# Optimization experiments

Hardware: AMD Instinct MI355X
Metric: run time of the kernel (lower is better)

## Reference

```python
import jax, jax.numpy as jnp
import numpy as np

N_NODES = 20000
N_EDGES = 320000
F_IN = 256      # feature_size
H1, C1 = 8, 128 # conv1: heads=8, out=128, concat -> 1024
H2, C2 = 1, 128 # conv2: heads=1, out=emb_size, concat=False
NEG_SLOPE = 0.2


def setup_inputs() -> dict:
    key = jax.random.key(0)
    ks = jax.random.split(key, 10)
    x = jax.random.normal(ks[0], (N_NODES, F_IN), dtype=jnp.float32)
    edge_index = jax.random.randint(ks[1], (2, N_EDGES), 0, N_NODES, dtype=jnp.int64)
    s1 = 1.0 / np.sqrt(F_IN)
    s2 = 1.0 / np.sqrt(H1 * C1)
    W1 = jax.random.uniform(ks[2], (F_IN, H1 * C1), jnp.float32, -s1, s1)
    att_src1 = jax.random.uniform(ks[3], (H1, C1), jnp.float32, -s1, s1)
    att_dst1 = jax.random.uniform(ks[4], (H1, C1), jnp.float32, -s1, s1)
    bias1 = jnp.zeros((H1 * C1,), jnp.float32)
    W2 = jax.random.uniform(ks[5], (H1 * C1, H2 * C2), jnp.float32, -s2, s2)
    att_src2 = jax.random.uniform(ks[6], (H2, C2), jnp.float32, -s2, s2)
    att_dst2 = jax.random.uniform(ks[7], (H2, C2), jnp.float32, -s2, s2)
    bias2 = jnp.zeros((C2,), jnp.float32)
    return {"x": x, "edge_index": edge_index,
            "W1": W1, "att_src1": att_src1, "att_dst1": att_dst1, "bias1": bias1,
            "W2": W2, "att_src2": att_src2, "att_dst2": att_dst2, "bias2": bias2}


def _gat_conv(x, W, a_src, a_dst, bias, src, dst, num_nodes, concat):
    """PyG-style GATConv (eval mode, self-loops already appended to src/dst)."""
    H, C = a_src.shape
    h = (x @ W).reshape(num_nodes, H, C)                     # [N,H,C]
    alpha_src = jnp.sum(h * a_src[None], axis=-1)            # [N,H]
    alpha_dst = jnp.sum(h * a_dst[None], axis=-1)            # [N,H]
    e = alpha_src[src] + alpha_dst[dst]                      # [E,H]
    e = jnp.where(e > 0, e, NEG_SLOPE * e)                   # LeakyReLU(0.2)
    # segment softmax over incoming edges of each dst node
    m = jax.ops.segment_max(e, dst, num_segments=num_nodes)  # [N,H]
    ex = jnp.exp(e - m[dst])
    denom = jax.ops.segment_sum(ex, dst, num_segments=num_nodes)
    alpha = ex / (denom[dst] + 1e-16)                        # [E,H]
    msg = alpha[:, :, None] * h[src]                         # [E,H,C]
    out = jax.ops.segment_sum(msg, dst, num_segments=num_nodes)  # [N,H,C]
    if concat:
        out = out.reshape(num_nodes, H * C)
    else:
        out = out.mean(axis=1)
    return out + bias


def reference(x, edge_index, W1, att_src1, att_dst1, bias1, W2, att_src2, att_dst2, bias2):
    n = x.shape[0]
    loop = jnp.arange(n, dtype=edge_index.dtype)
    src = jnp.concatenate([edge_index[0], loop])
    dst = jnp.concatenate([edge_index[1], loop])
    # dropout layers are identity in eval mode
    h = _gat_conv(x, W1, att_src1, att_dst1, bias1, src, dst, n, concat=True)
    h = jax.nn.elu(h)
    h = _gat_conv(h, W2, att_src2, att_dst2, bias2, src, dst, n, concat=False)
    return jax.nn.log_softmax(h, axis=-1)
```

## Files before the change

kernel.cpp:

```cpp
#include <hip/hip_runtime.h>

#define NN 20000
#define FIN 256
#define D1 1024
#define NH 8
#define C2 128
#define CAP 64

typedef unsigned short u16;
typedef unsigned char u8;
typedef __attribute__((ext_vector_type(8))) short bf16x8;
typedef __attribute__((ext_vector_type(4))) float f32x4;
typedef __attribute__((ext_vector_type(2))) float f32x2;

__device__ __forceinline__ float bf2f(u16 u) {
    return __uint_as_float(((unsigned int)u) << 16);
}
__device__ __forceinline__ u16 f2bf(float f) {
    unsigned int u = __float_as_uint(f);
    u += 0x7FFFu + ((u >> 16) & 1u);
    return (u16)(u >> 16);
}
__device__ __forceinline__ u8 f2fp8(float v) {
    int q = __builtin_amdgcn_cvt_pk_fp8_f32(v, v, 0, false);
    return (u8)(q & 0xFF);
}

__device__ __forceinline__ float bred_max(float v) {
    #pragma unroll
    for (int o = 32; o > 0; o >>= 1) v = fmaxf(v, __shfl_xor(v, o, 64));
    return v;
}
__device__ __forceinline__ float bred_sum(float v) {
    #pragma unroll
    for (int o = 32; o > 0; o >>= 1) v += __shfl_xor(v, o, 64);
    return v;
}

typedef const __attribute__((address_space(1))) unsigned int* as1_u32p;
typedef __attribute__((address_space(3))) unsigned int* as3_u32p;
__device__ __forceinline__ void gload_lds16(const void* g, void* l) {
    __builtin_amdgcn_global_load_lds((as1_u32p)g, (as3_u32p)l, 16, 0, 0);
}

__global__ __launch_bounds__(256) void prep_kernel(const float* __restrict__ x,
                                                   u16* __restrict__ xb,
                                                   const float* __restrict__ W1,
                                                   u16* __restrict__ w1t,
                                                   const float* __restrict__ W2,
                                                   u16* __restrict__ w2t,
                                                   int* __restrict__ cnt) {
    __shared__ float tile[32][33];
    const int b = blockIdx.x, tid = threadIdx.x;
    if (b < 5000) {
        int i = (b * 256 + tid) * 4;
        if (i < NN * FIN) {
            float4 v = *(const float4*)(x + i);
            ushort4 o;
            o.x = f2bf(v.x); o.y = f2bf(v.y); o.z = f2bf(v.z); o.w = f2bf(v.w);
            *(ushort4*)(xb + i) = o;
        }
        return;
    }
    if (b < 5384) {
        const float* in; u16* out; int R, C, bx, by;
        if (b < 5256) {
            int q = b - 5000;
            in = W1; out = w1t; R = FIN; C = D1;
            bx = (q & 31) * 32; by = (q >> 5) * 32;
        } else {
            int q = b - 5256;
            in = W2; out = w2t; R = D1; C = C2;
            bx = (q & 3) * 32; by = (q >> 2) * 32;
        }
        int tx = tid & 31, ty = tid >> 5;
        #pragma unroll
        for (int i = 0; i < 32; i += 8)
            tile[ty + i][tx] = in[(size_t)(by + ty + i) * C + bx + tx];
        __syncthreads();
        #pragma unroll
        for (int i = 0; i < 32; i += 8)
            out[(size_t)(bx + ty + i) * R + by + tx] = f2bf(tile[tx][ty + i]);
        return;
    }
    int i = (b - 5384) * 256 + tid;
    if (i < NN) cnt[i] = 0;
}

#define G_STAGE(BUF, K0)                                                   \
    {                                                                      \
        _Pragma("unroll")                                                  \
        for (int i = 0; i < BM / 64; i++) {                                \
            int c = tid + i * 256;                                         \
            int r = c >> 2, ko = (c & 3) * 8;                              \
            int gr = row0 + r; if (gr >= M) gr = M - 1;                    \
            gload_lds16(A + (size_t)gr * K + (K0) + ko,                    \
                        &ldsA[BUF][c * 8]);                                \
        }                                                                  \
        _Pragma("unroll")                                                  \
        for (int i = 0; i < 2; i++) {                                      \
            int c = tid + i * 256;                                         \
            int n = c >> 2, ko = (c & 3) * 8;                              \
            gload_lds16(Bt + (size_t)(col0 + n) * K + (K0) + ko,           \
                        &ldsB[BUF][c * 8]);                                \
        }                                                                  \
    }

template <int BM, int OMODE>
__global__ __launch_bounds__(256) void gemm_mfma(const u16* __restrict__ A,
                                                 const u16* __restrict__ Bt,
                                                 void* __restrict__ C,
                                                 const float* __restrict__ attS,
                                                 const float* __restrict__ attD,
                                                 float* __restrict__ as_out,
                                                 float* __restrict__ ad_out,
                                                 int NHo,
                                                 int M, int N, int K) {
    constexpr int TM = BM / 32;
    __shared__ u16 ldsA[2][BM * 32];
    __shared__ u16 ldsB[2][128 * 32];
    __shared__ float asb[BM], adb[BM];
    const int tid = threadIdx.x;
    const int lane = tid & 63, w = tid >> 6;
    const int wr = w >> 1, wc = w & 1;
    const int row0 = blockIdx.x * BM, col0 = blockIdx.y * 128;
    const int head = blockIdx.y;
    const int l15 = lane & 15, quad = lane >> 4;

    for (int t = tid; t < BM; t += 256) { asb[t] = 0.f; adb[t] = 0.f; }

    f32x4 acc[TM][4];
    #pragma unroll
    for (int i = 0; i < TM; i++)
        #pragma unroll
        for (int j = 0; j < 4; j++)
            acc[i][j] = (f32x4){0.f, 0.f, 0.f, 0.f};

    G_STAGE(0, 0)
    __syncthreads();
    int cur = 0;
    for (int k0 = 0; k0 < K; k0 += 32) {
        if (k0 + 32 < K) {
            G_STAGE(cur ^ 1, k0 + 32)
            __builtin_amdgcn_sched_barrier(0);
        }
        bf16x8 af[TM], bfr[4];
        #pragma unroll
        for (int i = 0; i < TM; i++) {
            int m = wr * (BM / 2) + i * 16 + l15;
            af[i] = *(const bf16x8*)(&ldsA[cur][m * 32 + quad * 8]);
        }
        #pragma unroll
        for (int j = 0; j < 4; j++) {
            int n = wc * 64 + j * 16 + l15;
            bfr[j] = *(const bf16x8*)(&ldsB[cur][n * 32 + quad * 8]);
        }
        #pragma unroll
        for (int i = 0; i < TM; i++)
            #pragma unroll
            for (int j = 0; j < 4; j++)
                acc[i][j] = __builtin_amdgcn_mfma_f32_16x16x32_bf16(af[i], bfr[j], acc[i][j], 0, 0, 0);
        __syncthreads();
        cur ^= 1;
    }
    #pragma unroll
    for (int i = 0; i < TM; i++) {
        #pragma unroll
        for (int j = 0; j < 4; j++) {
            #pragma unroll
            for (int r = 0; r < 4; r++) {
                int row = row0 + wr * (BM / 2) + i * 16 + quad * 4 + r;
                int col = col0 + wc * 64 + j * 16 + l15;
                if (row < M) {
                    float v = acc[i][j][r];
                    if (OMODE == 1)
                        ((u16*)C)[(size_t)row * N + col] = f2bf(v);
                    else
                        ((u8*)C)[(size_t)row * N + col] = f2fp8(v);
                }
            }
        }
    }
    float attS_r[4], attD_r[4];
    #pragma unroll
    for (int j = 0; j < 4; j++) {
        int col = wc * 64 + j * 16 + l15;
        attS_r[j] = attS[head * 128 + col];
        attD_r[j] = attD[head * 128 + col];
    }
    #pragma unroll
    for (int i = 0; i < TM; i++) {
        #pragma unroll
        for (int r = 0; r < 4; r++) {
            float ps = 0.f, pd = 0.f;
            #pragma unroll
            for (int j = 0; j < 4; j++) {
                float v = acc[i][j][r];
                ps = fmaf(v, attS_r[j], ps);
                pd = fmaf(v, attD_r[j], pd);
            }
            #pragma unroll
            for (int o = 1; o < 16; o <<= 1) {
                ps += __shfl_xor(ps, o, 64);
                pd += __shfl_xor(pd, o, 64);
            }
            if (l15 == 0) {
                int row = wr * (BM / 2) + i * 16 + quad * 4 + r;
                atomicAdd(&asb[row], ps);
                atomicAdd(&adb[row], pd);
            }
        }
    }
    __syncthreads();
    for (int t = tid; t < BM; t += 256) {
        int row = row0 + t;
        if (row < M) {
            as_out[(size_t)row * NHo + head] = asb[t];
            ad_out[(size_t)row * NHo + head] = adb[t];
        }
    }
}

__global__ void fill_kernel(const int* __restrict__ ei, int E, int N,
                            int* __restrict__ cnt,
                            int* __restrict__ csr) {
    int j = blockIdx.x * 256 + threadIdx.x;
    if (j >= E + N) return;
    int s, d;
    if (j < E) { s = ei[j]; d = ei[E + j]; }
    else { s = j - E; d = j - E; }
    int pos = atomicAdd(&cnt[d], 1);
    if (pos >= CAP) return;
    csr[d * CAP + pos] = s;
}

#define A1_FETCH8(E0, Q, P)                                                   \
    {                                                                         \
        _Pragma("unroll")                                                     \
        for (int u = 0; u < 8; u++) {                                         \
            int e = (E0) + u;                       \
            int s = __builtin_amdgcn_readlane(idx, e);                        \
            s = s < 0 ? 0 : (s > NN - 1 ? NN - 1 : s);        \
            Q[u] = *(const uint4*)(h1q + (size_t)s * D1 + c0);                \
            P[u] = as1[s * NH + h];            \
        }                                                                     \
        __builtin_amdgcn_sched_barrier(0);                                    \
    }
#define A1_PROC8(E0, Q, P)                                                    \
    {                                                                         \
        _Pragma("unroll")                                                     \
        for (int u = 0; u < 8; u++) {                                         \
            float ev = (P)[u] + adv;                                          \
            ev = ev > 0.f ? ev : 0.2f * ev;               \
            float pp = ((E0) + u < deg) ? __expf(ev) : 0.f;                   \
            den += pp;                                                        \
            f32x2 pv2 = {pp, pp};                                             \
            acc[0] += pv2 * __builtin_amdgcn_cvt_pk_f32_fp8((Q)[u].x, false); \
            acc[1] += pv2 * __builtin_amdgcn_cvt_pk_f32_fp8((Q)[u].x, true);  \
            acc[2] += pv2 * __builtin_amdgcn_cvt_pk_f32_fp8((Q)[u].y, false); \
            acc[3] += pv2 * __builtin_amdgcn_cvt_pk_f32_fp8((Q)[u].y, true);  \
            acc[4] += pv2 * __builtin_amdgcn_cvt_pk_f32_fp8((Q)[u].z, false); \
            acc[5] += pv2 * __builtin_amdgcn_cvt_pk_f32_fp8((Q)[u].z, true);  \
            acc[6] += pv2 * __builtin_amdgcn_cvt_pk_f32_fp8((Q)[u].w, false); \
            acc[7] += pv2 * __builtin_amdgcn_cvt_pk_f32_fp8((Q)[u].w, true);  \
        }                                                                     \
    }

__global__ __launch_bounds__(256) void agg1_kernel(const u8* __restrict__ h1q,
                                                   const float* __restrict__ as1,
                                                   const float* __restrict__ ad1,
                                                   const int* __restrict__ cnt,
                                                   const int* __restrict__ csr,
                                                   const float* __restrict__ bias1,
                                                   u16* __restrict__ x2) {
    const int tid = threadIdx.x;
    const int lane = tid & 63;
    const int dst = (blockIdx.x << 2) + (tid >> 6);
    const int c0 = lane * 16;
    const int h = lane >> 3;
    const int base = dst * CAP;

    int idx = csr[base + lane];
    const int deg = __builtin_amdgcn_readfirstlane(max(1, min(cnt[dst], CAP)));
    const float adv = ad1[dst * NH + h];

    f32x2 acc[8];
    #pragma unroll
    for (int k = 0; k < 8; k++) acc[k] = (f32x2){0.f, 0.f};
    float den = 0.f;

    const int nit = (deg + 7) >> 3;
    uint4 qa[8], qb[8];
    float pa[8], pb[8];
    A1_FETCH8(0, qa, pa)
    int g = 0;
    for (; g + 2 < nit; g += 2) {
        A1_FETCH8((g + 1) * 8, qb, pb)
        A1_PROC8(g * 8, qa, pa)
        A1_FETCH8((g + 2) * 8, qa, pa)
        A1_PROC8((g + 1) * 8, qb, pb)
    }
    if (g + 1 < nit) {
        A1_FETCH8((g + 1) * 8, qb, pb)
        A1_PROC8(g * 8, qa, pa)
        A1_PROC8((g + 1) * 8, qb, pb)
    } else {
        A1_PROC8(g * 8, qa, pa)
    }

    float inv = 1.f / (den + 1e-16f);
    u16 ov[16];
    #pragma unroll
    for (int k = 0; k < 8; k++) {
        float a0 = acc[k][0] * inv + bias1[c0 + 2 * k];
        float a1 = acc[k][1] * inv + bias1[c0 + 2 * k + 1];
        a0 = a0 > 0.f ? a0 : (__expf(a0) - 1.f);
        a1 = a1 > 0.f ? a1 : (__expf(a1) - 1.f);
        ov[2 * k] = f2bf(a0);
        ov[2 * k + 1] = f2bf(a1);
    }
    *(uint4*)(x2 + (size_t)dst * D1 + c0) = *(const uint4*)ov;
    *(uint4*)(x2 + (size_t)dst * D1 + c0 + 8) = *(const uint4*)(ov + 8);
}

#define A2_FETCH8(E0, Q)                                                      \
    {                                                                         \
        _Pragma("unroll")                                                     \
        for (int u = 0; u < 8; u++) {                                         \
            int s = __builtin_amdgcn_readlane(idx, (E0) + u);                 \
            s = s < 0 ? 0 : (s > NN - 1 ? NN - 1 : s);                        \
            Q[u] = *(const unsigned int*)(h2 + (size_t)s * C2 + lane2);       \
        }                                                                     \
        __builtin_amdgcn_sched_barrier(0);                                    \
    }
#define A2_PROC8(E0, Q)                                                       \
    {                                                                         \
        _Pragma("unroll")                                                     \
        for (int u = 0; u < 8; u++) {                                         \
            int e = (E0) + u;                                                 \
            float pp = (e < deg) ? __uint_as_float(__builtin_amdgcn_readlane( \
                                       __float_as_uint(pl), e))               \
                                 : 0.f;                                       \
            den += pp;                                                        \
            f32x2 pv2 = {pp, pp};                                             \
            f32x2 f = {__uint_as_float((Q)[u] << 16),                         \
                       __uint_as_float((Q)[u] & 0xFFFF0000u)};                \
            acc += pv2 * f;                                                   \
        }                                                                     \
    }

__global__ __launch_bounds__(256) void agg2_kernel(const u16* __restrict__ h2,
                                                   const float* __restrict__ as2,
                                                   const float* __restrict__ ad2,
                                                   const int* __restrict__ cnt,
                                                   const int* __restrict__ csr,
                                                   const float* __restrict__ bias2,
                                                   float* __restrict__ out) {
    const int tid = threadIdx.x;
    const int lane = tid & 63;
    const int dst = (blockIdx.x << 2) + (tid >> 6);
    const int base = dst * CAP;
    const int lane2 = lane * 2;

    int idx = csr[base + lane];
    const int deg = __builtin_amdgcn_readfirstlane(max(1, min(cnt[dst], CAP)));
    const float adv = ad2[dst];
    int idxc = idx < 0 ? 0 : (idx > NN - 1 ? NN - 1 : idx);
    float ev = as2[idxc] + adv;
    ev = ev > 0.f ? ev : 0.2f * ev;
    float pl = __expf(ev);

    f32x2 acc = {0.f, 0.f};
    float den = 0.f;

    const int nit = (deg + 7) >> 3;
    unsigned int qa[8], qb[8];
    A2_FETCH8(0, qa)
    int g = 0;
    for (; g + 2 < nit; g += 2) {
        A2_FETCH8((g + 1) * 8, qb)
        A2_PROC8(g * 8, qa)
        A2_FETCH8((g + 2) * 8, qa)
        A2_PROC8((g + 1) * 8, qb)
    }
    if (g + 1 < nit) {
        A2_FETCH8((g + 1) * 8, qb)
        A2_PROC8(g * 8, qa)
        A2_PROC8((g + 1) * 8, qb)
    } else {
        A2_PROC8(g * 8, qa)
    }

    float inv = 1.f / (den + 1e-16f);
    float l0 = acc[0] * inv + bias2[lane2];
    float l1 = acc[1] * inv + bias2[lane2 + 1];
    float m = bred_max(fmaxf(l0, l1));
    float ex = bred_sum(__expf(l0 - m) + __expf(l1 - m));
    float lse = m + __logf(ex);
    float2 ov = {l0 - lse, l1 - lse};
    *(float2*)(out + (size_t)dst * C2 + lane2) = ov;
}

extern "C" void kernel_launch(void* const* d_in, const int* in_sizes, int n_in,
                              void* d_out, int out_size, void* d_ws, size_t ws_size,
                              hipStream_t stream) {
    const float* x        = (const float*)d_in[0];
    const int*   ei       = (const int*)d_in[1];
    const float* W1       = (const float*)d_in[2];
    const float* att_src1 = (const float*)d_in[3];
    const float* att_dst1 = (const float*)d_in[4];
    const float* bias1    = (const float*)d_in[5];
    const float* W2       = (const float*)d_in[6];
    const float* att_src2 = (const float*)d_in[7];
    const float* att_dst2 = (const float*)d_in[8];
    const float* bias2    = (const float*)d_in[9];
    float* out = (float*)d_out;
    const int E = in_sizes[1] / 2;

    char* ws = (char*)d_ws;
    size_t off = 0;
    auto alloc = [&](size_t b) {
        void* p = ws + off;
        off += (b + 255) & ~(size_t)255;
        return p;
    };
    u8*  h1q  = (u8*)alloc((size_t)NN * D1);
    u16* x2   = (u16*)alloc((size_t)NN * D1 * 2);
    u16* h2   = (u16*)alloc((size_t)NN * C2 * 2);
    u16* xb   = (u16*)alloc((size_t)NN * FIN * 2);
    u16* w1t  = (u16*)alloc((size_t)D1 * FIN * 2);
    u16* w2t  = (u16*)alloc((size_t)C2 * D1 * 2);
    float* as1 = (float*)alloc((size_t)NN * NH * 4);
    float* ad1 = (float*)alloc((size_t)NN * NH * 4);
    float* as2 = (float*)alloc((size_t)NN * 4);
    float* ad2 = (float*)alloc((size_t)NN * 4);
    int* cnt  = (int*)alloc((size_t)NN * 4);
    int* csr  = (int*)alloc((size_t)NN * CAP * 4);

    const int PREP_BLOCKS = 5000 + 256 + 128 + (NN + 255) / 256;
    prep_kernel<<<PREP_BLOCKS, 256, 0, stream>>>(x, xb, W1, w1t, W2, w2t, cnt);

    gemm_mfma<128, 2><<<dim3((NN + 127) / 128, D1 / 128), 256, 0, stream>>>(
        xb, w1t, h1q, att_src1, att_dst1, as1, ad1, NH, NN, D1, FIN);
    fill_kernel<<<(E + NN + 255) / 256, 256, 0, stream>>>(ei, E, NN, cnt, csr);
    agg1_kernel<<<(NN + 3) / 4, 256, 0, stream>>>(h1q, as1, ad1, cnt, csr, bias1, x2);
    gemm_mfma<64, 1><<<dim3((NN + 63) / 64, C2 / 128), 256, 0, stream>>>(
        x2, w2t, h2, att_src2, att_dst2, as2, ad2, 1, NN, C2, D1);
    agg2_kernel<<<(NN + 3) / 4, 256, 0, stream>>>(h2, as2, ad2, cnt, csr, bias2, out);
}
```

Baseline: 231.2 us.

## Split layer-1 aggregation per head and fuse CSR fill into prep kernel

Layer-1 aggregation now launches 8x more blocks, one per (dst-group, head). Each wave handles one head's 128 columns, with each lane gathering 2 fp8 values per edge. Each lane computes one edge's attention weight up front, and the weights are broadcast with readlane, so per-edge exp and as1 loads are no longer repeated. The CSR fill kernel is folded into the prep kernel, and cnt is zeroed by a memset instead. The per-head split aims to raise parallelism and occupancy, but each gather is now a narrow 2-byte load and the csr/cnt reads are repeated eight times per node.

Result: slower. 260.0 us (+12.5%).

```diff
diff --git a/kernel.cpp b/kernel.cpp
--- a/kernel.cpp
+++ b/kernel.cpp
@@ -49,7 +49,10 @@
                                                    u16* __restrict__ w1t,
                                                    const float* __restrict__ W2,
                                                    u16* __restrict__ w2t,
-                                                   int* __restrict__ cnt) {
+                                                   const int* __restrict__ ei,
+                                                   int E,
+                                                   int* __restrict__ cnt,
+                                                   int* __restrict__ csr) {
     __shared__ float tile[32][33];
     const int b = blockIdx.x, tid = threadIdx.x;
     if (b < 5000) {
@@ -83,8 +86,14 @@
             out[(size_t)(bx + ty + i) * R + by + tx] = f2bf(tile[tx][ty + i]);
         return;
     }
-    int i = (b - 5384) * 256 + tid;
-    if (i < NN) cnt[i] = 0;
+    int j = (b - 5384) * 256 + tid;
+    if (j >= E + NN) return;
+    int s, d;
+    if (j < E) { s = ei[j]; d = ei[E + j]; }
+    else { s = j - E; d = j - E; }
+    int pos = atomicAdd(&cnt[d], 1);
+    if (pos >= CAP) return;
+    csr[d * CAP + pos] = s;
 }
 
 #define G_STAGE(BUF, K0)                                                   \
@@ -221,48 +230,28 @@
     }
 }
 
-__global__ void fill_kernel(const int* __restrict__ ei, int E, int N,
-                            int* __restrict__ cnt,
-                            int* __restrict__ csr) {
-    int j = blockIdx.x * 256 + threadIdx.x;
-    if (j >= E + N) return;
-    int s, d;
-    if (j < E) { s = ei[j]; d = ei[E + j]; }
-    else { s = j - E; d = j - E; }
-    int pos = atomicAdd(&cnt[d], 1);
-    if (pos >= CAP) return;
-    csr[d * CAP + pos] = s;
-}
-
-#define A1_FETCH8(E0, Q, P)                                                   \
+#define A1_FETCH8(E0, Q)                                                      \
     {                                                                         \
         _Pragma("unroll")                                                     \
         for (int u = 0; u < 8; u++) {                                         \
-            int e = (E0) + u;                       \
-            int s = __builtin_amdgcn_readlane(idx, e);                        \
+            int s = __builtin_amdgcn_readlane(idx, (E0) + u);                 \
             s = s < 0 ? 0 : (s > NN - 1 ? NN - 1 : s);        \
-            Q[u] = *(const uint4*)(h1q + (size_t)s * D1 + c0);                \
-            P[u] = as1[s * NH + h];            \
+            Q[u] = *(const u16*)(h1q + (size_t)s * D1 + coff);                \
         }                                                                     \
         __builtin_amdgcn_sched_barrier(0);                                    \
     }
-#define A1_PROC8(E0, Q, P)                                                    \
+#define A1_PROC8(E0, Q)                                                       \
     {                                                                         \
         _Pragma("unroll")                                                     \
         for (int u = 0; u < 8; u++) {                                         \
-            float ev = (P)[u] + adv;                                          \
-            ev = ev > 0.f ? ev : 0.2f * ev;               \
-            float pp = ((E0) + u < deg) ? __expf(ev) : 0.f;                   \
+            int e = (E0) + u;                                                 \
+            float pp = (e < deg) ? __uint_as_float(__builtin_amdgcn_readlane( \
+                                       __float_as_uint(pl), e))               \
+                                 : 0.f;                                       \
             den += pp;                                                        \
             f32x2 pv2 = {pp, pp};                                             \
-            acc[0] += pv2 * __builtin_amdgcn_cvt_pk_f32_fp8((Q)[u].x, false); \
-            acc[1] += pv2 * __builtin_amdgcn_cvt_pk_f32_fp8((Q)[u].x, true);  \
-            acc[2] += pv2 * __builtin_amdgcn_cvt_pk_f32_fp8((Q)[u].y, false); \
-            acc[3] += pv2 * __builtin_amdgcn_cvt_pk_f32_fp8((Q)[u].y, true);  \
-            acc[4] += pv2 * __builtin_amdgcn_cvt_pk_f32_fp8((Q)[u].z, false); \
-            acc[5] += pv2 * __builtin_amdgcn_cvt_pk_f32_fp8((Q)[u].z, true);  \
-            acc[6] += pv2 * __builtin_amdgcn_cvt_pk_f32_fp8((Q)[u].w, false); \
-            acc[7] += pv2 * __builtin_amdgcn_cvt_pk_f32_fp8((Q)[u].w, true);  \
+            acc += pv2 * __builtin_amdgcn_cvt_pk_f32_fp8((unsigned int)(Q)[u],\
+                                                         false);              \
         }                                                                     \
     }
 
@@ -275,52 +264,48 @@
                                                    u16* __restrict__ x2) {
     const int tid = threadIdx.x;
     const int lane = tid & 63;
-    const int dst = (blockIdx.x << 2) + (tid >> 6);
-    const int c0 = lane * 16;
-    const int h = lane >> 3;
+    const int sl = blockIdx.x & 7;
+    const int dst = ((blockIdx.x >> 3) << 2) + (tid >> 6);
     const int base = dst * CAP;
+    const int coff = sl * 128 + lane * 2;
 
     int idx = csr[base + lane];
     const int deg = __builtin_amdgcn_readfirstlane(max(1, min(cnt[dst], CAP)));
-    const float adv = ad1[dst * NH + h];
-
-    f32x2 acc[8];
-    #pragma unroll
-    for (int k = 0; k < 8; k++) acc[k] = (f32x2){0.f, 0.f};
+    const float adv = ad1[dst * NH + sl];
+    int idxc = idx < 0 ? 0 : (idx > NN - 1 ? NN - 1 : idx);
+    float ev = as1[idxc * NH + sl] + adv;
+    ev = ev > 0.f ? ev : 0.2f * ev;
+    float pl = __expf(ev);
+
+    f32x2 acc = {0.f, 0.f};
     float den = 0.f;
 
     const int nit = (deg + 7) >> 3;
-    uint4 qa[8], qb[8];
-    float pa[8], pb[8];
-    A1_FETCH8(0, qa, pa)
+    u16 qa[8], qb[8];
+    A1_FETCH8(0, qa)
     int g = 0;
     for (; g + 2 < nit; g += 2) {
-        A1_FETCH8((g + 1) * 8, qb, pb)
-        A1_PROC8(g * 8, qa, pa)
-        A1_FETCH8((g + 2) * 8, qa, pa)
-        A1_PROC8((g + 1) * 8, qb, pb)
+        A1_FETCH8((g + 1) * 8, qb)
+        A1_PROC8(g * 8, qa)
+        A1_FETCH8((g + 2) * 8, qa)
+        A1_PROC8((g + 1) * 8, qb)
     }
     if (g + 1 < nit) {
-        A1_FETCH8((g + 1) * 8, qb, pb)
-        A1_PROC8(g * 8, qa, pa)
-        A1_PROC8((g + 1) * 8, qb, pb)
+        A1_FETCH8((g + 1) * 8, qb)
+        A1_PROC8(g * 8, qa)
+        A1_PROC8((g + 1) * 8, qb)
     } else {
-        A1_PROC8(g * 8, qa, pa)
+        A1_PROC8(g * 8, qa)
     }
 
     float inv = 1.f / (den + 1e-16f);
-    u16 ov[16];
-    #pragma unroll
-    for (int k = 0; k < 8; k++) {
-        float a0 = acc[k][0] * inv + bias1[c0 + 2 * k];
-        float a1 = acc[k][1] * inv + bias1[c0 + 2 * k + 1];
-        a0 = a0 > 0.f ? a0 : (__expf(a0) - 1.f);
-        a1 = a1 > 0.f ? a1 : (__expf(a1) - 1.f);
-        ov[2 * k] = f2bf(a0);
-        ov[2 * k + 1] = f2bf(a1);
-    }
-    *(uint4*)(x2 + (size_t)dst * D1 + c0) = *(const uint4*)ov;
-    *(uint4*)(x2 + (size_t)dst * D1 + c0 + 8) = *(const uint4*)(ov + 8);
+    float2 bv = *(const float2*)(bias1 + coff);
+    float a0 = acc[0] * inv + bv.x;
+    float a1 = acc[1] * inv + bv.y;
+    a0 = a0 > 0.f ? a0 : (__expf(a0) - 1.f);
+    a1 = a1 > 0.f ? a1 : (__expf(a1) - 1.f);
+    unsigned int ow = (unsigned int)f2bf(a0) | ((unsigned int)f2bf(a1) << 16);
+    *(unsigned int*)(x2 + (size_t)dst * D1 + coff) = ow;
 }
 
 #define A2_FETCH8(E0, Q)                                                      \
@@ -437,13 +422,15 @@
     int* cnt  = (int*)alloc((size_t)NN * 4);
     int* csr  = (int*)alloc((size_t)NN * CAP * 4);
 
-    const int PREP_BLOCKS = 5000 + 256 + 128 + (NN + 255) / 256;
-    prep_kernel<<<PREP_BLOCKS, 256, 0, stream>>>(x, xb, W1, w1t, W2, w2t, cnt);
+    hipMemsetAsync(cnt, 0, (size_t)NN * 4, stream);
+    const int FILL_BLOCKS = (E + NN + 255) / 256;
+    prep_kernel<<<5384 + FILL_BLOCKS, 256, 0, stream>>>(x, xb, W1, w1t, W2, w2t,
+                                                        ei, E, cnt, csr);
 
     gemm_mfma<128, 2><<<dim3((NN + 127) / 128, D1 / 128), 256, 0, stream>>>(
         xb, w1t, h1q, att_src1, att_dst1, as1, ad1, NH, NN, D1, FIN);
-    fill_kernel<<<(E + NN + 255) / 256, 256, 0, stream>>>(ei, E, NN, cnt, csr);
-    agg1_kernel<<<(NN + 3) / 4, 256, 0, stream>>>(h1q, as1, ad1, cnt, csr, bias1, x2);
+    agg1_kernel<<<((NN + 3) / 4) * 8, 256, 0, stream>>>(h1q, as1, ad1, cnt, csr,
+                                                        bias1, x2);
     gemm_mfma<64, 1><<<dim3((NN + 63) / 64, C2 / 128), 256, 0, stream>>>(
         x2, w2t, h2, att_src2, att_dst2, as2, ad2, 1, NN, C2, D1);
     agg2_kernel<<<(NN + 3) / 4, 256, 0, stream>>>(h2, as2, ad2, cnt, csr, bias2, out);
```
